# Kernel optimization log

Measured on AMD Instinct MI355X. Metric: run time of the kernel, lower is better.

The kernel has to match this reference:

```python
import jax, jax.numpy as jnp
import numpy as np

B, N, K = 8, 1024, 1024
C1, C2 = 64, 128
EPS = 1e-5
XTOL = 1e-7


def _skew(w):
    x, y, z = w[..., 0], w[..., 1], w[..., 2]
    o = jnp.zeros_like(x)
    r0 = jnp.stack([o, -z, y], axis=-1)
    r1 = jnp.stack([z, o, -x], axis=-1)
    r2 = jnp.stack([-y, x, o], axis=-1)
    return jnp.stack([r0, r1, r2], axis=-2)


def _expmap(dx):
    # se(3) exponential map, twist = [w(3), v(3)] -> [B,4,4]
    w, v = dx[:, :3], dx[:, 3:]
    t = jnp.linalg.norm(w, axis=1)
    W = _skew(w)
    S = jnp.matmul(W, W)
    t2 = t * t
    small = t < 1e-4
    ts = jnp.where(small, jnp.ones_like(t), t)
    s1 = jnp.where(small, 1.0 - t2 / 6.0, jnp.sin(ts) / ts)            # sin(t)/t
    s2 = jnp.where(small, 0.5 - t2 / 24.0, (1.0 - jnp.cos(ts)) / (ts * ts))  # (1-cos t)/t^2
    s3 = jnp.where(small, 1.0 / 6.0 - t2 / 120.0, (ts - jnp.sin(ts)) / (ts * ts * ts))  # (t-sin t)/t^3
    I = jnp.eye(3, dtype=dx.dtype)
    R = I + s1[:, None, None] * W + s2[:, None, None] * S
    V = I + s2[:, None, None] * W + s3[:, None, None] * S
    p = jnp.einsum('bij,bj->bi', V, v)
    g = jnp.zeros((dx.shape[0], 4, 4), dtype=dx.dtype)
    g = g.at[:, :3, :3].set(R).at[:, :3, 3].set(p).at[:, 3, 3].set(1.0)
    return g


def _transform(g, p):
    # g: [B,4,4] rigid transforms, p: [B,N,3]
    return jnp.einsum('bij,bnj->bni', g[:, :3, :3], p) + g[:, None, :3, 3]


def _bn_eval(x, gamma, beta, rm, rv_):
    # eval-mode batchnorm over channel dim of [B,C,N]
    return gamma[:, None] * (x - rm[:, None]) * jax.lax.rsqrt(rv_[:, None] + EPS) + beta[:, None]


def _pointnet(p, params, with_jac=False):
    # shared-MLP PointNet: conv1x1 -> BN(eval) -> ReLU (x3), then max-pool over points
    x = jnp.swapaxes(p, 1, 2)  # [B,3,N]
    masks = []
    for (Wt, b, gamma, beta, rm, rv_) in params:
        x = jnp.einsum('oc,bcn->bon', Wt, x) + b[:, None]
        x = _bn_eval(x, gamma, beta, rm, rv_)
        x = jnp.maximum(x, 0.0)
        if with_jac:
            masks.append((x > 0.0).astype(x.dtype))
    f = jnp.max(x, axis=-1)  # [B,K]
    if with_jac:
        return f, masks, jnp.argmax(x, axis=-1)  # max_idx [B,K]
    return f


def _cal_pinv(p0, params, masks, max_idx):
    # analytical Jacobian (Cal_Jac) + Gauss-Newton pseudo-inverse
    bsz, npts = p0.shape[0], p0.shape[1]
    W1, W2, W3 = params[0][0], params[1][0], params[2][0]
    d1 = params[0][2] * jax.lax.rsqrt(params[0][5] + EPS)  # dBN/dx in eval mode (per channel)
    d2 = params[1][2] * jax.lax.rsqrt(params[1][5] + EPS)
    d3 = params[2][2] * jax.lax.rsqrt(params[2][5] + EPS)
    D1 = d1[None, :, None] * masks[0]  # [B,C1,N]
    D2 = d2[None, :, None] * masks[1]  # [B,C2,N]
    D3 = d3[None, :, None] * masks[2]  # [B,K,N]
    # feature jacobian chain d f / d p : [B,K,N,3]
    t1 = jnp.einsum('ci,bcn->bnic', W1, D1)            # [B,N,3,C1]
    t2 = jnp.einsum('bnic,dc,bdn->bnid', t1, W2, D2)   # [B,N,3,C2]
    fj = jnp.einsum('bnid,kd,bkn->bkni', t2, W3, D3)   # [B,K,N,3]
    # warp jacobian at identity twist: [-[p]x | -I3] -> [B,N,3,6]
    eye3 = jnp.broadcast_to(jnp.eye(3, dtype=p0.dtype), (bsz, npts, 3, 3))
    warp = jnp.concatenate([-_skew(p0), -eye3], axis=-1)
    # gather the argmax point per feature channel (only rows surviving max-pool)
    fjg = jnp.take_along_axis(fj, max_idx[:, :, None, None], axis=2)[:, :, 0, :]  # [B,K,3]
    wg = jnp.take_along_axis(warp.reshape(bsz, npts, 18), max_idx[:, :, None], axis=1)
    wg = wg.reshape(bsz, -1, 3, 6)  # [B,K,3,6]
    J = jnp.einsum('bki,bkim->bkm', fjg, wg)  # [B,K,6]
    H = jnp.einsum('bki,bkj->bij', J, J)      # [B,6,6]
    pinv = jnp.einsum('bij,bkj->bik', jnp.linalg.inv(H), J)  # [B,6,K]
    return pinv


def _forward(p0, p1, W1, b1, gamma1, beta1, rm1, rv1, W2, b2, gamma2, beta2, rm2, rv2, W3, b3, gamma3, beta3, rm3, rv3, maxiter):
    params = [(W1, b1, gamma1, beta1, rm1, rv1),
              (W2, b2, gamma2, beta2, rm2, rv2),
              (W3, b3, gamma3, beta3, rm3, rv3)]
    f0, masks, max_idx = _pointnet(p0, params, with_jac=True)
    pinv = _cal_pinv(p0, params, masks, max_idx)
    bsz = p0.shape[0]
    g0 = jnp.broadcast_to(jnp.eye(4, dtype=p0.dtype), (bsz, 4, 4))

    def step(carry, _):
        g, r, done = carry
        p = _transform(g, p1)
        f = _pointnet(p, params)
        r_new = jnp.where(done, r, f - f0)           # freeze residual after xtol break
        dx = jnp.einsum('bik,bk->bi', pinv, r_new)   # Gauss-Newton step [B,6]
        conv = jnp.max(jnp.linalg.norm(dx, axis=1)) < XTOL
        stop = done | conv
        g_new = jnp.where(stop, g, jnp.matmul(_expmap(dx), g))
        return (g_new, r_new, stop), None

    init = (g0, jnp.zeros_like(f0), jnp.array(False))
    (g, r, _), _ = jax.lax.scan(step, init, None, length=maxiter)
    return r


def setup_inputs():
    key = jax.random.key(0)
    ks = jax.random.split(key, 24)
    f32 = jnp.float32
    rn = lambda i, s, sc=1.0: jax.random.normal(ks[i], s, dtype=f32) * sc
    ru = lambda i, s: jax.random.uniform(ks[i], s, dtype=f32, minval=0.5, maxval=1.5)
    p0 = rn(0, (B, N, 3))
    inp = {
        'p0': p0,
        'p1': p0 + rn(1, (B, N, 3), 0.02),  # small rigid-ish perturbation -> meaningful registration
        'W1': rn(2, (C1, 3), 0.5), 'b1': rn(3, (C1,), 0.1),
        'gamma1': ru(4, (C1,)), 'beta1': rn(5, (C1,), 0.1),
        'rm1': rn(6, (C1,), 0.1), 'rv1': ru(7, (C1,)),
        'W2': rn(8, (C2, C1), 0.2), 'b2': rn(9, (C2,), 0.1),
        'gamma2': ru(10, (C2,)), 'beta2': rn(11, (C2,), 0.1),
        'rm2': rn(12, (C2,), 0.1), 'rv2': ru(13, (C2,)),
        'W3': rn(14, (K, C2), 0.1), 'b3': rn(15, (K,), 0.1),
        'gamma3': ru(16, (K,)), 'beta3': rn(17, (K,), 0.1),
        'rm3': rn(18, (K,), 0.1), 'rv3': ru(19, (K,)),
        'maxiter': 10,
    }
    return inp


def reference(p0, p1, W1, b1, gamma1, beta1, rm1, rv1, W2, b2, gamma2, beta2, rm2, rv2, W3, b3, gamma3, beta3, rm3, rv3, maxiter):
    return _forward(p0, p1, W1, b1, gamma1, beta1, rm1, rv1, W2, b2, gamma2, beta2, rm2, rv2, W3, b3, gamma3, beta3, rm3, rv3, maxiter)
```

## Files before the change

kernel.cpp:

```cpp
#include <hip/hip_runtime.h>

#define B_ 8
#define N_ 1024
#define C1_ 64
#define C2_ 128
#define K_ 1024
#define EPS_ 1e-5f
#define XTOL_ 1e-7f

#define OFF_G      0
#define OFF_F0     128
#define OFF_PM     8320
#define OFF_M1     24704
#define OFF_M2     41088
#define OFF_SC3    73856
#define OFF_OFF3   74880
#define OFF_OFF2   75904
#define OFF_W1F    76032
#define OFF_W3HI   76288
#define OFF_W3LO   141824
#define OFF_W2H    207360
#define OFF_W2L    211456
#define OFF_J      215552
#define OFF_PINVT  264704
#define OFF_PART   330240
#define OFF_DXG    461312
#define OFF_NRM    461360
#define OFF_CNT    461368

typedef __attribute__((ext_vector_type(8))) short bf16x8;
typedef __attribute__((ext_vector_type(4))) float f32x4;

static __device__ inline unsigned short f2bf(float x) {
    unsigned u = __float_as_uint(x);
    unsigned r = (u + 0x7FFFu + ((u >> 16) & 1u)) >> 16;
    return (unsigned short)r;
}
static __device__ inline float bf2f(unsigned short h) {
    return __uint_as_float(((unsigned)h) << 16);
}
static __device__ inline unsigned pk2(unsigned short a, unsigned short b) {
    return (unsigned)a | ((unsigned)b << 16);
}

__global__ __launch_bounds__(256)
void k_prep(const float* __restrict__ W3, const float* __restrict__ b3,
            const float* __restrict__ ga3, const float* __restrict__ be3,
            const float* __restrict__ rm3, const float* __restrict__ rv3,
            const float* __restrict__ W1, const float* __restrict__ b1,
            const float* __restrict__ ga1, const float* __restrict__ be1,
            const float* __restrict__ rm1, const float* __restrict__ rv1,
            const float* __restrict__ W2, const float* __restrict__ b2,
            const float* __restrict__ ga2, const float* __restrict__ be2,
            const float* __restrict__ rm2, const float* __restrict__ rv2,
            unsigned short* __restrict__ w3hi, unsigned short* __restrict__ w3lo,
            float* __restrict__ sc3, float* __restrict__ off3,
            unsigned short* __restrict__ w2h, unsigned short* __restrict__ w2l,
            float* __restrict__ off2, float* __restrict__ w1f,
            unsigned int* __restrict__ cnt) {
    int gid = blockIdx.x * 256 + threadIdx.x;
    if (gid < K_ * C2_) {
        float w = W3[gid];
        unsigned short h = f2bf(w);
        w3hi[gid] = h;
        w3lo[gid] = f2bf(w - bf2f(h));
    }
    if (gid < K_) {
        float sc = ga3[gid] * rsqrtf(rv3[gid] + EPS_);
        sc3[gid] = sc;
        off3[gid] = sc * (b3[gid] - rm3[gid]) + be3[gid];
    }
    if (gid < C2_ * C1_) {
        int o = gid >> 6, c = gid & 63;
        float sc = ga2[o] * rsqrtf(rv2[o] + EPS_);
        float v = W2[o * C1_ + c] * sc;
        unsigned short h = f2bf(v);
        w2h[o * C1_ + c] = h;
        w2l[o * C1_ + c] = f2bf(v - bf2f(h));
    }
    if (gid < C2_) {
        float sc = ga2[gid] * rsqrtf(rv2[gid] + EPS_);
        off2[gid] = sc * (b2[gid] - rm2[gid]) + be2[gid];
    }
    if (gid < C1_) {
        float sc = ga1[gid] * rsqrtf(rv1[gid] + EPS_);
        w1f[gid * 4 + 0] = W1[gid * 3 + 0] * sc;
        w1f[gid * 4 + 1] = W1[gid * 3 + 1] * sc;
        w1f[gid * 4 + 2] = W1[gid * 3 + 2] * sc;
        w1f[gid * 4 + 3] = sc * (b1[gid] - rm1[gid]) + be1[gid];
    }
    if (gid == 0) *cnt = 0u;
}

template<int MODE>
__global__ __launch_bounds__(512, 2)
void k_fused(const float* __restrict__ pts, const float* __restrict__ g,
             const float* __restrict__ w1f,
             const unsigned short* __restrict__ w2h, const unsigned short* __restrict__ w2l,
             const float* __restrict__ off2,
             const unsigned short* __restrict__ w3hi, const unsigned short* __restrict__ w3lo,
             const float* __restrict__ sc3, const float* __restrict__ off3,
             unsigned long long* __restrict__ part,
             unsigned long long* __restrict__ m1b, unsigned int* __restrict__ m2q) {
    __shared__ __align__(16) unsigned short a1h[128][72];
    __shared__ __align__(16) unsigned short a1l[128][72];
    __shared__ __align__(16) unsigned short sB[2][128][136];
    __shared__ float sSc[256], sOff[256], sOff2[C2_];
    __shared__ unsigned int m1w[2][128];
    __shared__ unsigned int m2w[4][128];
    __shared__ unsigned long long pmL[256];

    int slab = blockIdx.x;
    int b    = blockIdx.y;
    int q    = blockIdx.z;
    int n0   = slab * 128;
    int tx   = threadIdx.x;
    int w    = tx >> 6;
    int l    = tx & 63;
    int l15  = l & 15;
    int lhi  = l >> 4;

    if (tx < 256) { sSc[tx] = sc3[q * 256 + tx]; sOff[tx] = off3[q * 256 + tx]; }
    if (tx < C2_) sOff2[tx] = off2[tx];
    if (MODE == 0 && tx < 128) {
        m1w[0][tx] = 0u; m1w[1][tx] = 0u;
        m2w[0][tx] = 0u; m2w[1][tx] = 0u; m2w[2][tx] = 0u; m2w[3][tx] = 0u;
    }
    __syncthreads();

    {
        int n = tx & 127;
        int cgi = tx >> 7;
        const float* pp = pts + (b * N_ + n0 + n) * 3;
        float px = pp[0], py = pp[1], pz = pp[2];
        float q0, q1, q2;
        if (MODE == 1) {
            const float* gb = g + b * 16;
            q0 = fmaf(gb[0], px, fmaf(gb[1], py, fmaf(gb[2],  pz, gb[3])));
            q1 = fmaf(gb[4], px, fmaf(gb[5], py, fmaf(gb[6],  pz, gb[7])));
            q2 = fmaf(gb[8], px, fmaf(gb[9], py, fmaf(gb[10], pz, gb[11])));
        } else {
            q0 = px; q1 = py; q2 = pz;
        }
        unsigned int bits = 0u;
        unsigned hw[8], lw[8];
        #pragma unroll
        for (int j = 0; j < 16; ++j) {
            int c = cgi * 16 + j;
            float4 wf = *(const float4*)(w1f + c * 4);
            float y = fmaxf(fmaf(wf.x, q0, fmaf(wf.y, q1, fmaf(wf.z, q2, wf.w))), 0.f);
            unsigned short h = f2bf(y);
            unsigned short lo = f2bf(y - bf2f(h));
            if (j & 1) { hw[j >> 1] |= ((unsigned)h) << 16; lw[j >> 1] |= ((unsigned)lo) << 16; }
            else       { hw[j >> 1] = (unsigned)h;          lw[j >> 1] = (unsigned)lo; }
            if (MODE == 0) bits |= ((unsigned int)(y > 0.f)) << j;
        }
        uint4 v0; v0.x = hw[0]; v0.y = hw[1]; v0.z = hw[2]; v0.w = hw[3];
        uint4 v1; v1.x = hw[4]; v1.y = hw[5]; v1.z = hw[6]; v1.w = hw[7];
        *(uint4*)&a1h[n][cgi * 16 + 0] = v0;
        *(uint4*)&a1h[n][cgi * 16 + 8] = v1;
        uint4 v2; v2.x = lw[0]; v2.y = lw[1]; v2.z = lw[2]; v2.w = lw[3];
        uint4 v3; v3.x = lw[4]; v3.y = lw[5]; v3.z = lw[6]; v3.w = lw[7];
        *(uint4*)&a1l[n][cgi * 16 + 0] = v2;
        *(uint4*)&a1l[n][cgi * 16 + 8] = v3;
        if (MODE == 0) atomicOr(&m1w[cgi >> 1][n], bits << ((cgi & 1) * 16));
    }
    __syncthreads();

    {
        f32x4 acc2[8];
        #pragma unroll
        for (int nf = 0; nf < 8; ++nf) acc2[nf] = (f32x4){0.f, 0.f, 0.f, 0.f};
        #pragma unroll
        for (int ks = 0; ks < 2; ++ks) {
            int k0 = ks * 32;
            int aoff = (w * 16 + l15) * C1_ + k0 + lhi * 8;
            bf16x8 ah2 = *(const bf16x8*)(w2h + aoff);
            bf16x8 al2 = *(const bf16x8*)(w2l + aoff);
            #pragma unroll
            for (int nf = 0; nf < 8; ++nf) {
                bf16x8 bh2 = *(const bf16x8*)&a1h[nf * 16 + l15][k0 + lhi * 8];
                bf16x8 bl2 = *(const bf16x8*)&a1l[nf * 16 + l15][k0 + lhi * 8];
                acc2[nf] = __builtin_amdgcn_mfma_f32_16x16x32_bf16(ah2, bh2, acc2[nf], 0, 0, 0);
                acc2[nf] = __builtin_amdgcn_mfma_f32_16x16x32_bf16(ah2, bl2, acc2[nf], 0, 0, 0);
                acc2[nf] = __builtin_amdgcn_mfma_f32_16x16x32_bf16(al2, bh2, acc2[nf], 0, 0, 0);
            }
        }
        #pragma unroll
        for (int nf = 0; nf < 8; ++nf) {
            int n = nf * 16 + l15;
            unsigned short h4[4], l4[4];
            #pragma unroll
            for (int r = 0; r < 4; ++r) {
                int o = w * 16 + lhi * 4 + r;
                float y = fmaxf(acc2[nf][r] + sOff2[o], 0.f);
                unsigned short h = f2bf(y);
                h4[r] = h;
                l4[r] = f2bf(y - bf2f(h));
                if (MODE == 0 && y > 0.f) atomicOr(&m2w[o >> 5][n], 1u << (o & 31));
            }
            uint2 vh; vh.x = pk2(h4[0], h4[1]); vh.y = pk2(h4[2], h4[3]);
            uint2 vl; vl.x = pk2(l4[0], l4[1]); vl.y = pk2(l4[2], l4[3]);
            *(uint2*)&sB[0][n][w * 16 + lhi * 4] = vh;
            *(uint2*)&sB[1][n][w * 16 + lhi * 4] = vl;
        }
    }
    __syncthreads();

    if (MODE == 0 && q == 0 && tx < 128) {
        m1b[b * N_ + n0 + tx] =
            (unsigned long long)m1w[0][tx] | ((unsigned long long)m1w[1][tx] << 32);
        uint4 mv; mv.x = m2w[0][tx]; mv.y = m2w[1][tx]; mv.z = m2w[2][tx]; mv.w = m2w[3][tx];
        *(uint4*)&m2q[(b * N_ + n0 + tx) * 4] = mv;
    }

    f32x4 acc[2][8];
    #pragma unroll
    for (int fi = 0; fi < 2; ++fi)
        #pragma unroll
        for (int nf = 0; nf < 8; ++nf) acc[fi][nf] = (f32x4){0.f, 0.f, 0.f, 0.f};

    #pragma unroll
    for (int ks = 0; ks < 4; ++ks) {
        int k0 = ks * 32;
        bf16x8 bh[8], bl[8];
        #pragma unroll
        for (int nf = 0; nf < 8; ++nf) {
            bh[nf] = *(const bf16x8*)&sB[0][nf * 16 + l15][k0 + lhi * 8];
            bl[nf] = *(const bf16x8*)&sB[1][nf * 16 + l15][k0 + lhi * 8];
        }
        #pragma unroll
        for (int fi = 0; fi < 2; ++fi) {
            int orow = q * 256 + w * 32 + fi * 16 + l15;
            int off = orow * C2_ + k0 + lhi * 8;
            bf16x8 ah = *(const bf16x8*)(w3hi + off);
            bf16x8 al = *(const bf16x8*)(w3lo + off);
            #pragma unroll
            for (int nf = 0; nf < 8; ++nf) {
                acc[fi][nf] = __builtin_amdgcn_mfma_f32_16x16x32_bf16(ah, bh[nf], acc[fi][nf], 0, 0, 0);
                acc[fi][nf] = __builtin_amdgcn_mfma_f32_16x16x32_bf16(ah, bl[nf], acc[fi][nf], 0, 0, 0);
                acc[fi][nf] = __builtin_amdgcn_mfma_f32_16x16x32_bf16(al, bh[nf], acc[fi][nf], 0, 0, 0);
            }
        }
    }

    #pragma unroll
    for (int fi = 0; fi < 2; ++fi) {
        #pragma unroll
        for (int r = 0; r < 4; ++r) {
            int o_l = w * 32 + fi * 16 + lhi * 4 + r;
            float sc = sSc[o_l], of = sOff[o_l];
            float bv = -3.4e38f;
            int bi = 0;
            #pragma unroll
            for (int nf = 0; nf < 8; ++nf) {
                float y = fmaxf(sc * acc[fi][nf][r] + of, 0.f);
                int nn = n0 + nf * 16 + l15;
                if (y > bv) { bv = y; bi = nn; }
            }
            #pragma unroll
            for (int m = 1; m <= 8; m <<= 1) {
                float ov = __shfl_xor(bv, m);
                int oi = __shfl_xor(bi, m);
                if (ov > bv || (ov == bv && oi < bi)) { bv = ov; bi = oi; }
            }
            if (l15 == 0) {
                pmL[o_l] = ((unsigned long long)__float_as_uint(bv) << 32)
                         | (unsigned int)(~(unsigned int)bi);
            }
        }
    }
    __syncthreads();
    if (tx < 256)
        part[(size_t)slab * (B_ * K_) + b * K_ + q * 256 + tx] = pmL[tx];
}

__global__ __launch_bounds__(256)
void k_reduce(const unsigned long long* __restrict__ part,
              unsigned long long* __restrict__ pm) {
    int gid = blockIdx.x * 256 + threadIdx.x;
    unsigned long long m = part[gid];
    #pragma unroll
    for (int s = 1; s < 8; ++s) {
        unsigned long long v = part[(size_t)s * (B_ * K_) + gid];
        m = (v > m) ? v : m;
    }
    pm[gid] = m;
}

__global__ __launch_bounds__(256)
void k_rdx(const unsigned long long* __restrict__ part,
           const float* __restrict__ f0, const float* __restrict__ pinvT,
           float* __restrict__ out, float* __restrict__ g,
           float* __restrict__ dxg, float* __restrict__ nrmg,
           unsigned int* __restrict__ cnt) {
    __shared__ float redB[4][6];
    __shared__ int isLast;
    int bb = blockIdx.x;
    int tx = threadIdx.x;
    int w = tx >> 6;
    int l = tx & 63;

    float acc[6] = {0.f, 0.f, 0.f, 0.f, 0.f, 0.f};
    #pragma unroll
    for (int half = 0; half < 4; ++half) {
        int o = half * 256 + tx;
        unsigned long long m = part[(size_t)bb * K_ + o];
        #pragma unroll
        for (int s = 1; s < 8; ++s) {
            unsigned long long v = part[(size_t)s * (B_ * K_) + bb * K_ + o];
            m = (v > m) ? v : m;
        }
        float fv = __uint_as_float((unsigned int)(m >> 32));
        float rv = fv - f0[bb * K_ + o];
        out[bb * K_ + o] = rv;
        const float4* pp = (const float4*)(pinvT + (size_t)(bb * K_ + o) * 8);
        float4 pa = pp[0], pb = pp[1];
        acc[0] += pa.x * rv; acc[1] += pa.y * rv; acc[2] += pa.z * rv;
        acc[3] += pa.w * rv; acc[4] += pb.x * rv; acc[5] += pb.y * rv;
    }
    #pragma unroll
    for (int i = 0; i < 6; ++i)
        for (int off = 32; off > 0; off >>= 1) acc[i] += __shfl_down(acc[i], off);
    if (l == 0) {
        #pragma unroll
        for (int i = 0; i < 6; ++i) redB[w][i] = acc[i];
    }
    __syncthreads();
    if (tx == 0) {
        float dx6[6];
        #pragma unroll
        for (int i = 0; i < 6; ++i) {
            dx6[i] = redB[0][i] + redB[1][i] + redB[2][i] + redB[3][i];
            atomicExch(&dxg[bb * 6 + i], dx6[i]);
        }
        atomicExch(&nrmg[bb],
                   sqrtf(dx6[0]*dx6[0] + dx6[1]*dx6[1] + dx6[2]*dx6[2]
                       + dx6[3]*dx6[3] + dx6[4]*dx6[4] + dx6[5]*dx6[5]));
    }
    __threadfence();
    __syncthreads();
    if (tx == 0) {
        unsigned int old = atomicAdd(cnt, 1u);
        isLast = (old == B_ - 1) ? 1 : 0;
        if (isLast) atomicExch(cnt, 0u);
    }
    __syncthreads();
    if (!isLast) return;

    if (tx < B_) {
        int b = tx;
        float mx = 0.f;
        #pragma unroll
        for (int i = 0; i < B_; ++i) mx = fmaxf(mx, atomicAdd(&nrmg[i], 0.f));
        if (mx < XTOL_) return;
        float d[6];
        #pragma unroll
        for (int i = 0; i < 6; ++i) d[i] = atomicAdd(&dxg[b * 6 + i], 0.f);
        float wx = d[0], wy = d[1], wz = d[2];
        float vx = d[3], vy = d[4], vz = d[5];
        float t2 = wx*wx + wy*wy + wz*wz;
        float t = sqrtf(t2);
        float s1, s2, s3;
        if (t < 1e-4f) {
            s1 = 1.f - t2 / 6.f;
            s2 = 0.5f - t2 / 24.f;
            s3 = 1.f / 6.f - t2 / 120.f;
        } else {
            float st = sinf(t), ct = cosf(t);
            s1 = st / t;
            s2 = (1.f - ct) / t2;
            s3 = (t - st) / (t2 * t);
        }
        float W[3][3] = {{0.f, -wz, wy}, {wz, 0.f, -wx}, {-wy, wx, 0.f}};
        float S[3][3];
        #pragma unroll
        for (int i = 0; i < 3; ++i)
            #pragma unroll
            for (int j = 0; j < 3; ++j)
                S[i][j] = W[i][0]*W[0][j] + W[i][1]*W[1][j] + W[i][2]*W[2][j];
        float R[3][3], V[3][3];
        #pragma unroll
        for (int i = 0; i < 3; ++i)
            #pragma unroll
            for (int j = 0; j < 3; ++j) {
                float id = (i == j) ? 1.f : 0.f;
                R[i][j] = id + s1 * W[i][j] + s2 * S[i][j];
                V[i][j] = id + s2 * W[i][j] + s3 * S[i][j];
            }
        float p[3];
        #pragma unroll
        for (int i = 0; i < 3; ++i) p[i] = V[i][0]*vx + V[i][1]*vy + V[i][2]*vz;
        float* gb = g + b * 16;
        float go[16];
        #pragma unroll
        for (int i = 0; i < 16; ++i) go[i] = gb[i];
        #pragma unroll
        for (int i = 0; i < 3; ++i)
            #pragma unroll
            for (int j = 0; j < 4; ++j)
                gb[i * 4 + j] = R[i][0]*go[0*4+j] + R[i][1]*go[1*4+j]
                              + R[i][2]*go[2*4+j] + p[i]*go[3*4+j];
    }
}

__global__ __launch_bounds__(256)
void k_jac(const float* __restrict__ p0,
           const unsigned long long* __restrict__ m1b,
           const unsigned int* __restrict__ m2q,
           const float* __restrict__ W1, const float* __restrict__ ga1, const float* __restrict__ rv1,
           const float* __restrict__ W2, const float* __restrict__ ga2, const float* __restrict__ rv2,
           const float* __restrict__ W3, const float* __restrict__ ga3, const float* __restrict__ rv3,
           const unsigned long long* __restrict__ pm,
           float* __restrict__ f0, float* __restrict__ J) {
    __shared__ float wvs[4][128];
    int tx = threadIdx.x;
    int wv = tx >> 6;
    int l = tx & 63;
    int w = blockIdx.x * 4 + wv;
    int b = w >> 10;
    int k = w & 1023;

    unsigned long long pk = pm[b * K_ + k];
    float f0v = __uint_as_float((unsigned int)(pk >> 32));
    int ns = (int)(~(unsigned int)pk);
    if (l == 0) f0[b * K_ + k] = f0v;

    unsigned long long m1 = m1b[b * N_ + ns];
    const unsigned int* mq = m2q + (b * N_ + ns) * 4;
    unsigned int qa = mq[0], qb = mq[1], qc = mq[2], qd = mq[3];
    unsigned int blo = (l < 32) ? (qa >> l) : (qb >> (l - 32));
    unsigned int bhi = (l < 32) ? (qc >> l) : (qd >> (l - 32));

    const float* w3r = W3 + k * C2_;
    float s2a = ga2[l] * rsqrtf(rv2[l] + EPS_);
    float s2b = ga2[64 + l] * rsqrtf(rv2[64 + l] + EPS_);
    float wa = (blo & 1u) ? w3r[l] * s2a : 0.f;
    float wb = (bhi & 1u) ? w3r[64 + l] * s2b : 0.f;
    wvs[wv][l] = wa;
    wvs[wv][64 + l] = wb;
    __syncthreads();

    float v = 0.f;
    #pragma unroll 8
    for (int d = 0; d < C2_; ++d) v += wvs[wv][d] * W2[d * C1_ + l];

    float d1l = ((m1 >> l) & 1ull) ? ga1[l] * rsqrtf(rv1[l] + EPS_) : 0.f;
    float vc = v * d1l;
    float fj0 = vc * W1[l * 3 + 0];
    float fj1 = vc * W1[l * 3 + 1];
    float fj2 = vc * W1[l * 3 + 2];
    #pragma unroll
    for (int off = 32; off; off >>= 1) {
        fj0 += __shfl_xor(fj0, off);
        fj1 += __shfl_xor(fj1, off);
        fj2 += __shfl_xor(fj2, off);
    }
    if (l == 0) {
        float D3 = (f0v > 0.f) ? ga3[k] * rsqrtf(rv3[k] + EPS_) : 0.f;
        fj0 *= D3; fj1 *= D3; fj2 *= D3;
        float x = p0[(b * N_ + ns) * 3 + 0];
        float y = p0[(b * N_ + ns) * 3 + 1];
        float z = p0[(b * N_ + ns) * 3 + 2];
        float* Jr = J + (b * K_ + k) * 6;
        Jr[0] = fj1 * (-z) + fj2 * y;
        Jr[1] = fj0 * z    + fj2 * (-x);
        Jr[2] = fj0 * (-y) + fj1 * x;
        Jr[3] = -fj0;
        Jr[4] = -fj1;
        Jr[5] = -fj2;
    }
}

__global__ void k_hpinv(const float* __restrict__ J, float* __restrict__ pinvT,
                        float* __restrict__ g) {
    int b = blockIdx.x;
    int tx = threadIdx.x;
    __shared__ float red[256][22];
    __shared__ float hinv[36];

    if (tx < 16) g[b * 16 + tx] = (tx % 5 == 0) ? 1.f : 0.f;

    float h[21];
    #pragma unroll
    for (int q = 0; q < 21; ++q) h[q] = 0.f;
    for (int k = tx; k < K_; k += 256) {
        const float* Jr = J + (b * K_ + k) * 6;
        float jv[6] = {Jr[0], Jr[1], Jr[2], Jr[3], Jr[4], Jr[5]};
        int q = 0;
        #pragma unroll
        for (int i = 0; i < 6; ++i)
            #pragma unroll
            for (int jj = i; jj < 6; ++jj) h[q++] += jv[i] * jv[jj];
    }
    #pragma unroll
    for (int q = 0; q < 21; ++q) red[tx][q] = h[q];
    __syncthreads();
    for (int s = 128; s > 0; s >>= 1) {
        if (tx < s)
            for (int q = 0; q < 21; ++q) red[tx][q] += red[tx + s][q];
        __syncthreads();
    }
    if (tx == 0) {
        float A[6][6], Inv[6][6];
        {
            int q = 0;
            #pragma unroll
            for (int i = 0; i < 6; ++i)
                #pragma unroll
                for (int jj = i; jj < 6; ++jj) { A[i][jj] = red[0][q]; A[jj][i] = red[0][q]; ++q; }
        }
        #pragma unroll
        for (int i = 0; i < 6; ++i)
            #pragma unroll
            for (int jj = 0; jj < 6; ++jj) Inv[i][jj] = (i == jj) ? 1.f : 0.f;
        #pragma unroll
        for (int col = 0; col < 6; ++col) {
            float ipv = 1.f / A[col][col];
            #pragma unroll
            for (int jj = 0; jj < 6; ++jj) { A[col][jj] *= ipv; Inv[col][jj] *= ipv; }
            #pragma unroll
            for (int r2 = 0; r2 < 6; ++r2) {
                if (r2 == col) continue;
                float f = A[r2][col];
                #pragma unroll
                for (int jj = 0; jj < 6; ++jj) {
                    A[r2][jj]   -= f * A[col][jj];
                    Inv[r2][jj] -= f * Inv[col][jj];
                }
            }
        }
        #pragma unroll
        for (int i = 0; i < 6; ++i)
            #pragma unroll
            for (int jj = 0; jj < 6; ++jj) hinv[i * 6 + jj] = Inv[i][jj];
    }
    __syncthreads();
    for (int k = tx; k < K_; k += 256) {
        const float* Jr = J + (b * K_ + k) * 6;
        float j0 = Jr[0], j1 = Jr[1], j2 = Jr[2], j3 = Jr[3], j4 = Jr[4], j5 = Jr[5];
        float* pr = pinvT + (b * K_ + k) * 8;
        #pragma unroll
        for (int i = 0; i < 6; ++i) {
            pr[i] = hinv[i * 6 + 0] * j0 + hinv[i * 6 + 1] * j1 + hinv[i * 6 + 2] * j2
                  + hinv[i * 6 + 3] * j3 + hinv[i * 6 + 4] * j4 + hinv[i * 6 + 5] * j5;
        }
        pr[6] = 0.f; pr[7] = 0.f;
    }
}

extern "C" void kernel_launch(void* const* d_in, const int* in_sizes, int n_in,
                              void* d_out, int out_size, void* d_ws, size_t ws_size,
                              hipStream_t stream) {
    const float* p0  = (const float*)d_in[0];
    const float* p1  = (const float*)d_in[1];
    const float* W1  = (const float*)d_in[2];
    const float* b1  = (const float*)d_in[3];
    const float* ga1 = (const float*)d_in[4];
    const float* be1 = (const float*)d_in[5];
    const float* rm1 = (const float*)d_in[6];
    const float* rv1 = (const float*)d_in[7];
    const float* W2  = (const float*)d_in[8];
    const float* b2  = (const float*)d_in[9];
    const float* ga2 = (const float*)d_in[10];
    const float* be2 = (const float*)d_in[11];
    const float* rm2 = (const float*)d_in[12];
    const float* rv2 = (const float*)d_in[13];
    const float* W3  = (const float*)d_in[14];
    const float* b3  = (const float*)d_in[15];
    const float* ga3 = (const float*)d_in[16];
    const float* be3 = (const float*)d_in[17];
    const float* rm3 = (const float*)d_in[18];
    const float* rv3 = (const float*)d_in[19];

    float* ws   = (float*)d_ws;
    float* g    = ws + OFF_G;
    float* f0   = ws + OFF_F0;
    unsigned long long* pm  = (unsigned long long*)(ws + OFF_PM);
    unsigned long long* m1b = (unsigned long long*)(ws + OFF_M1);
    unsigned int*       m2q = (unsigned int*)(ws + OFF_M2);
    float* sc3  = ws + OFF_SC3;
    float* off3 = ws + OFF_OFF3;
    float* off2 = ws + OFF_OFF2;
    float* w1f  = ws + OFF_W1F;
    unsigned short* w3hi = (unsigned short*)(ws + OFF_W3HI);
    unsigned short* w3lo = (unsigned short*)(ws + OFF_W3LO);
    unsigned short* w2h  = (unsigned short*)(ws + OFF_W2H);
    unsigned short* w2l  = (unsigned short*)(ws + OFF_W2L);
    float* Jb    = ws + OFF_J;
    float* pinvT = ws + OFF_PINVT;
    unsigned long long* part = (unsigned long long*)(ws + OFF_PART);
    float* dxg   = ws + OFF_DXG;
    float* nrmg  = ws + OFF_NRM;
    unsigned int* cnt = (unsigned int*)(ws + OFF_CNT);
    float* out   = (float*)d_out;

    dim3 gridF(8, B_, 4);

    k_prep<<<(K_ * C2_ + 255) / 256, 256, 0, stream>>>(
        W3, b3, ga3, be3, rm3, rv3,
        W1, b1, ga1, be1, rm1, rv1,
        W2, b2, ga2, be2, rm2, rv2,
        w3hi, w3lo, sc3, off3, w2h, w2l, off2, w1f, cnt);

    k_fused<0><<<gridF, 512, 0, stream>>>(p0, g, w1f, w2h, w2l, off2, w3hi, w3lo,
                                          sc3, off3, part, m1b, m2q);
    k_reduce<<<B_ * K_ / 256, 256, 0, stream>>>(part, pm);
    k_jac<<<B_ * K_ / 4, 256, 0, stream>>>(p0, m1b, m2q, W1, ga1, rv1, W2, ga2, rv2,
                                           W3, ga3, rv3, pm, f0, Jb);
    k_hpinv<<<B_, 256, 0, stream>>>(Jb, pinvT, g);

    for (int it = 0; it < 10; ++it) {
        k_fused<1><<<gridF, 512, 0, stream>>>(p1, g, w1f, w2h, w2l, off2, w3hi, w3lo,
                                              sc3, off3, part, m1b, m2q);
        k_rdx<<<B_, 256, 0, stream>>>(part, f0, pinvT, out, g, dxg, nrmg, cnt);
    }
}
```

Measured before the change: 277.6 us.

## Double block size of fused PointNet kernel to halve per-warp work

Raises the fused kernel from 512 to 1024 threads per block and re-partitions every stage. Layer-1 work now covers 8 channels per thread, layer-2 MFMA tiles are split across two point halves, and layer-3 gives each warp one 16-row output tile instead of two. The aim is more waves per CU and fewer accumulator registers per thread, to better hide latency. In exchange, per-wave reuse of the shared B fragments and W3 loads drops. Launch bounds of (1024,4) put heavy pressure on the register budget and may cause spills.

Result: faster. 257.7 us (median of 3 runs) (-7.2%).

```diff
diff --git a/kernel.cpp b/kernel.cpp
--- a/kernel.cpp
+++ b/kernel.cpp
@@ -93,7 +93,7 @@
 }
 
 template<int MODE>
-__global__ __launch_bounds__(512, 2)
+__global__ __launch_bounds__(1024, 4)
 void k_fused(const float* __restrict__ pts, const float* __restrict__ g,
              const float* __restrict__ w1f,
              const unsigned short* __restrict__ w2h, const unsigned short* __restrict__ w2l,
@@ -143,10 +143,10 @@
             q0 = px; q1 = py; q2 = pz;
         }
         unsigned int bits = 0u;
-        unsigned hw[8], lw[8];
-        #pragma unroll
-        for (int j = 0; j < 16; ++j) {
-            int c = cgi * 16 + j;
+        unsigned hw[4], lw[4];
+        #pragma unroll
+        for (int j = 0; j < 8; ++j) {
+            int c = cgi * 8 + j;
             float4 wf = *(const float4*)(w1f + c * 4);
             float y = fmaxf(fmaf(wf.x, q0, fmaf(wf.y, q1, fmaf(wf.z, q2, wf.w))), 0.f);
             unsigned short h = f2bf(y);
@@ -155,45 +155,44 @@
             else       { hw[j >> 1] = (unsigned)h;          lw[j >> 1] = (unsigned)lo; }
             if (MODE == 0) bits |= ((unsigned int)(y > 0.f)) << j;
         }
-        uint4 v0; v0.x = hw[0]; v0.y = hw[1]; v0.z = hw[2]; v0.w = hw[3];
-        uint4 v1; v1.x = hw[4]; v1.y = hw[5]; v1.z = hw[6]; v1.w = hw[7];
-        *(uint4*)&a1h[n][cgi * 16 + 0] = v0;
-        *(uint4*)&a1h[n][cgi * 16 + 8] = v1;
-        uint4 v2; v2.x = lw[0]; v2.y = lw[1]; v2.z = lw[2]; v2.w = lw[3];
-        uint4 v3; v3.x = lw[4]; v3.y = lw[5]; v3.z = lw[6]; v3.w = lw[7];
-        *(uint4*)&a1l[n][cgi * 16 + 0] = v2;
-        *(uint4*)&a1l[n][cgi * 16 + 8] = v3;
-        if (MODE == 0) atomicOr(&m1w[cgi >> 1][n], bits << ((cgi & 1) * 16));
+        uint4 vh; vh.x = hw[0]; vh.y = hw[1]; vh.z = hw[2]; vh.w = hw[3];
+        uint4 vl; vl.x = lw[0]; vl.y = lw[1]; vl.z = lw[2]; vl.w = lw[3];
+        *(uint4*)&a1h[n][cgi * 8] = vh;
+        *(uint4*)&a1l[n][cgi * 8] = vl;
+        if (MODE == 0) atomicOr(&m1w[cgi >> 2][n], bits << ((cgi & 3) * 8));
     }
     __syncthreads();
 
     {
-        f32x4 acc2[8];
-        #pragma unroll
-        for (int nf = 0; nf < 8; ++nf) acc2[nf] = (f32x4){0.f, 0.f, 0.f, 0.f};
+        int og = w & 7;
+        int nh = (w >> 3) * 4;
+        f32x4 acc2[4];
+        #pragma unroll
+        for (int nfi = 0; nfi < 4; ++nfi) acc2[nfi] = (f32x4){0.f, 0.f, 0.f, 0.f};
         #pragma unroll
         for (int ks = 0; ks < 2; ++ks) {
             int k0 = ks * 32;
-            int aoff = (w * 16 + l15) * C1_ + k0 + lhi * 8;
+            int aoff = (og * 16 + l15) * C1_ + k0 + lhi * 8;
             bf16x8 ah2 = *(const bf16x8*)(w2h + aoff);
             bf16x8 al2 = *(const bf16x8*)(w2l + aoff);
             #pragma unroll
-            for (int nf = 0; nf < 8; ++nf) {
-                bf16x8 bh2 = *(const bf16x8*)&a1h[nf * 16 + l15][k0 + lhi * 8];
-                bf16x8 bl2 = *(const bf16x8*)&a1l[nf * 16 + l15][k0 + lhi * 8];
-                acc2[nf] = __builtin_amdgcn_mfma_f32_16x16x32_bf16(ah2, bh2, acc2[nf], 0, 0, 0);
-                acc2[nf] = __builtin_amdgcn_mfma_f32_16x16x32_bf16(ah2, bl2, acc2[nf], 0, 0, 0);
-                acc2[nf] = __builtin_amdgcn_mfma_f32_16x16x32_bf16(al2, bh2, acc2[nf], 0, 0, 0);
+            for (int nfi = 0; nfi < 4; ++nfi) {
+                int n = (nh + nfi) * 16 + l15;
+                bf16x8 bh2 = *(const bf16x8*)&a1h[n][k0 + lhi * 8];
+                bf16x8 bl2 = *(const bf16x8*)&a1l[n][k0 + lhi * 8];
+                acc2[nfi] = __builtin_amdgcn_mfma_f32_16x16x32_bf16(ah2, bh2, acc2[nfi], 0, 0, 0);
+                acc2[nfi] = __builtin_amdgcn_mfma_f32_16x16x32_bf16(ah2, bl2, acc2[nfi], 0, 0, 0);
+                acc2[nfi] = __builtin_amdgcn_mfma_f32_16x16x32_bf16(al2, bh2, acc2[nfi], 0, 0, 0);
             }
         }
         #pragma unroll
-        for (int nf = 0; nf < 8; ++nf) {
-            int n = nf * 16 + l15;
+        for (int nfi = 0; nfi < 4; ++nfi) {
+            int n = (nh + nfi) * 16 + l15;
             unsigned short h4[4], l4[4];
             #pragma unroll
             for (int r = 0; r < 4; ++r) {
-                int o = w * 16 + lhi * 4 + r;
-                float y = fmaxf(acc2[nf][r] + sOff2[o], 0.f);
+                int o = og * 16 + lhi * 4 + r;
+                float y = fmaxf(acc2[nfi][r] + sOff2[o], 0.f);
                 unsigned short h = f2bf(y);
                 h4[r] = h;
                 l4[r] = f2bf(y - bf2f(h));
@@ -201,8 +200,8 @@
             }
             uint2 vh; vh.x = pk2(h4[0], h4[1]); vh.y = pk2(h4[2], h4[3]);
             uint2 vl; vl.x = pk2(l4[0], l4[1]); vl.y = pk2(l4[2], l4[3]);
-            *(uint2*)&sB[0][n][w * 16 + lhi * 4] = vh;
-            *(uint2*)&sB[1][n][w * 16 + lhi * 4] = vl;
+            *(uint2*)&sB[0][n][og * 16 + lhi * 4] = vh;
+            *(uint2*)&sB[1][n][og * 16 + lhi * 4] = vl;
         }
     }
     __syncthreads();
@@ -214,60 +213,57 @@
         *(uint4*)&m2q[(b * N_ + n0 + tx) * 4] = mv;
     }
 
-    f32x4 acc[2][8];
-    #pragma unroll
-    for (int fi = 0; fi < 2; ++fi)
-        #pragma unroll
-        for (int nf = 0; nf < 8; ++nf) acc[fi][nf] = (f32x4){0.f, 0.f, 0.f, 0.f};
+    f32x4 acc[8];
+    #pragma unroll
+    for (int nf = 0; nf < 8; ++nf) acc[nf] = (f32x4){0.f, 0.f, 0.f, 0.f};
 
     #pragma unroll
     for (int ks = 0; ks < 4; ++ks) {
         int k0 = ks * 32;
-        bf16x8 bh[8], bl[8];
+        int orow = q * 256 + w * 16 + l15;
+        int off = orow * C2_ + k0 + lhi * 8;
+        bf16x8 ah = *(const bf16x8*)(w3hi + off);
+        bf16x8 al = *(const bf16x8*)(w3lo + off);
+        #pragma unroll
+        for (int nh = 0; nh < 2; ++nh) {
+            bf16x8 bh[4], bl[4];
+            #pragma unroll
+            for (int nfi = 0; nfi < 4; ++nfi) {
+                int n = (nh * 4 + nfi) * 16 + l15;
+                bh[nfi] = *(const bf16x8*)&sB[0][n][k0 + lhi * 8];
+                bl[nfi] = *(const bf16x8*)&sB[1][n][k0 + lhi * 8];
+            }
+            #pragma unroll
+            for (int nfi = 0; nfi < 4; ++nfi) {
+                int nf = nh * 4 + nfi;
+                acc[nf] = __builtin_amdgcn_mfma_f32_16x16x32_bf16(ah, bh[nfi], acc[nf], 0, 0, 0);
+                acc[nf] = __builtin_amdgcn_mfma_f32_16x16x32_bf16(ah, bl[nfi], acc[nf], 0, 0, 0);
+                acc[nf] = __builtin_amdgcn_mfma_f32_16x16x32_bf16(al, bh[nfi], acc[nf], 0, 0, 0);
+            }
+        }
+    }
+
+    #pragma unroll
+    for (int r = 0; r < 4; ++r) {
+        int o_l = w * 16 + lhi * 4 + r;
+        float sc = sSc[o_l], of = sOff[o_l];
+        float bv = -3.4e38f;
+        int bi = 0;
         #pragma unroll
         for (int nf = 0; nf < 8; ++nf) {
-            bh[nf] = *(const bf16x8*)&sB[0][nf * 16 + l15][k0 + lhi * 8];
-            bl[nf] = *(const bf16x8*)&sB[1][nf * 16 + l15][k0 + lhi * 8];
-        }
-        #pragma unroll
-        for (int fi = 0; fi < 2; ++fi) {
-            int orow = q * 256 + w * 32 + fi * 16 + l15;
-            int off = orow * C2_ + k0 + lhi * 8;
-            bf16x8 ah = *(const bf16x8*)(w3hi + off);
-            bf16x8 al = *(const bf16x8*)(w3lo + off);
-            #pragma unroll
-            for (int nf = 0; nf < 8; ++nf) {
-                acc[fi][nf] = __builtin_amdgcn_mfma_f32_16x16x32_bf16(ah, bh[nf], acc[fi][nf], 0, 0, 0);
-                acc[fi][nf] = __builtin_amdgcn_mfma_f32_16x16x32_bf16(ah, bl[nf], acc[fi][nf], 0, 0, 0);
-                acc[fi][nf] = __builtin_amdgcn_mfma_f32_16x16x32_bf16(al, bh[nf], acc[fi][nf], 0, 0, 0);
-            }
-        }
-    }
-
-    #pragma unroll
-    for (int fi = 0; fi < 2; ++fi) {
-        #pragma unroll
-        for (int r = 0; r < 4; ++r) {
-            int o_l = w * 32 + fi * 16 + lhi * 4 + r;
-            float sc = sSc[o_l], of = sOff[o_l];
-            float bv = -3.4e38f;
-            int bi = 0;
-            #pragma unroll
-            for (int nf = 0; nf < 8; ++nf) {
-                float y = fmaxf(sc * acc[fi][nf][r] + of, 0.f);
-                int nn = n0 + nf * 16 + l15;
-                if (y > bv) { bv = y; bi = nn; }
-            }
-            #pragma unroll
-            for (int m = 1; m <= 8; m <<= 1) {
-                float ov = __shfl_xor(bv, m);
-                int oi = __shfl_xor(bi, m);
-                if (ov > bv || (ov == bv && oi < bi)) { bv = ov; bi = oi; }
-            }
-            if (l15 == 0) {
-                pmL[o_l] = ((unsigned long long)__float_as_uint(bv) << 32)
-                         | (unsigned int)(~(unsigned int)bi);
-            }
+            float y = fmaxf(sc * acc[nf][r] + of, 0.f);
+            int nn = n0 + nf * 16 + l15;
+            if (y > bv) { bv = y; bi = nn; }
+        }
+        #pragma unroll
+        for (int m = 1; m <= 8; m <<= 1) {
+            float ov = __shfl_xor(bv, m);
+            int oi = __shfl_xor(bi, m);
+            if (ov > bv || (ov == bv && oi < bi)) { bv = ov; bi = oi; }
+        }
+        if (l15 == 0) {
+            pmL[o_l] = ((unsigned long long)__float_as_uint(bv) << 32)
+                     | (unsigned int)(~(unsigned int)bi);
         }
     }
     __syncthreads();
@@ -603,16 +599,16 @@
         W2, b2, ga2, be2, rm2, rv2,
         w3hi, w3lo, sc3, off3, w2h, w2l, off2, w1f, cnt);
 
-    k_fused<0><<<gridF, 512, 0, stream>>>(p0, g, w1f, w2h, w2l, off2, w3hi, w3lo,
-                                          sc3, off3, part, m1b, m2q);
+    k_fused<0><<<gridF, 1024, 0, stream>>>(p0, g, w1f, w2h, w2l, off2, w3hi, w3lo,
+                                           sc3, off3, part, m1b, m2q);
     k_reduce<<<B_ * K_ / 256, 256, 0, stream>>>(part, pm);
     k_jac<<<B_ * K_ / 4, 256, 0, stream>>>(p0, m1b, m2q, W1, ga1, rv1, W2, ga2, rv2,
                                            W3, ga3, rv3, pm, f0, Jb);
     k_hpinv<<<B_, 256, 0, stream>>>(Jb, pinvT, g);
 
     for (int it = 0; it < 10; ++it) {
-        k_fused<1><<<gridF, 512, 0, stream>>>(p1, g, w1f, w2h, w2l, off2, w3hi, w3lo,
-                                              sc3, off3, part, m1b, m2q);
+        k_fused<1><<<gridF, 1024, 0, stream>>>(p1, g, w1f, w2h, w2l, off2, w3hi, w3lo,
+                                               sc3, off3, part, m1b, m2q);
         k_rdx<<<B_, 256, 0, stream>>>(part, f0, pinvT, out, g, dxg, nrmg, cnt);
     }
 }
```
